# Performance work log

Measured on AMD Instinct MI355X. Metric: run time of the kernel, lower is better.

The kernel has to match this reference:

```python
import jax, jax.numpy as jnp
import numpy as np

TOP_K_FREQ = 16


def setup_inputs() -> dict:
    key = jax.random.key(0)
    x = jax.random.normal(key, (64, 4096, 128), dtype=jnp.float32)
    return {"x": x}


def reference(x):
    B, L, C = x.shape
    freq = jnp.fft.rfft(x, axis=1)              # [B, F, C] complex, F = L//2 + 1
    F = freq.shape[1]
    k = min(TOP_K_FREQ, F)
    mag = jnp.abs(freq)                          # [B, F, C]
    # top-k over frequency axis, vectorized across (B, C)
    mag_bcf = jnp.transpose(mag, (0, 2, 1))      # [B, C, F]
    _, idx = jax.lax.top_k(mag_bcf, k)           # idx: [B, C, k]
    b_ix = jnp.arange(B)[:, None, None]
    c_ix = jnp.arange(C)[None, :, None]
    mask_bcf = jnp.zeros((B, C, F), dtype=x.dtype).at[b_ix, c_ix, idx].set(1.0)
    mask = jnp.transpose(mask_bcf, (0, 2, 1))    # [B, F, C]
    freq_filtered = freq * mask
    out = jnp.fft.irfft(freq_filtered, n=L, axis=1)  # [B, L, C]
    return out.astype(x.dtype)
```

## Files before the change

kernel.cpp:

```cpp
#include <hip/hip_runtime.h>


#define SWZ(i) ((i) ^ (((i) >> 4) & 15))

__device__ __forceinline__ int drev8(int x) {
  return ((x & 7) << 9) | ((x & 0x38) << 3) | ((x >> 3) & 0x38) | ((x >> 9) & 7);
}

__device__ __forceinline__ float2 cmulf(float2 a, float c, float s) {
  return make_float2(a.x * c - a.y * s, a.x * s + a.y * c);
}

__device__ __forceinline__ float2 cadd(float2 a, float2 b) { return make_float2(a.x + b.x, a.y + b.y); }
__device__ __forceinline__ float2 csub(float2 a, float2 b) { return make_float2(a.x - b.x, a.y - b.y); }
__device__ __forceinline__ float2 cmulnegi(float2 a) { return make_float2(a.y, -a.x); }
__device__ __forceinline__ float2 cmulposi(float2 a) { return make_float2(-a.y, a.x); }

__device__ __forceinline__ void dft8(float2* a) {
  const float R = 0.7071067811865476f;
  float2 t0 = cadd(a[0], a[4]), t1 = cadd(a[1], a[5]);
  float2 t2 = cadd(a[2], a[6]), t3 = cadd(a[3], a[7]);
  float2 u0 = csub(a[0], a[4]);
  float2 d1 = csub(a[1], a[5]);
  float2 u1 = make_float2(R * (d1.x + d1.y), R * (d1.y - d1.x));
  float2 u2 = cmulnegi(csub(a[2], a[6]));
  float2 d3 = csub(a[3], a[7]);
  float2 u3 = make_float2(R * (d3.y - d3.x), R * (-(d3.x + d3.y)));
  {
    float2 b0 = cadd(t0, t2), b1 = csub(t0, t2);
    float2 b2 = cadd(t1, t3), b3 = csub(t1, t3);
    a[0] = cadd(b0, b2);
    a[2] = cadd(b1, cmulnegi(b3));
    a[4] = csub(b0, b2);
    a[6] = cadd(b1, cmulposi(b3));
  }
  {
    float2 b0 = cadd(u0, u2), b1 = csub(u0, u2);
    float2 b2 = cadd(u1, u3), b3 = csub(u1, u3);
    a[1] = cadd(b0, b2);
    a[3] = cadd(b1, cmulnegi(b3));
    a[5] = csub(b0, b2);
    a[7] = cadd(b1, cmulposi(b3));
  }
}

template <int STRIDE, int M>
__device__ __forceinline__ void fft_pass8(float2* Zl, int base, int j) {
  float2 v[8];
  #pragma unroll
  for (int p = 0; p < 8; p++) v[p] = Zl[SWZ(base + j + STRIDE * p)];
  dft8(v);
  #pragma unroll
  for (int r = 1; r < 8; r++) {
    if (M > 8) {
      int a = j * r;
      float x = (float)a * (1.0f / (float)M);
      float s = -__builtin_amdgcn_sinf(x);
      float c =  __builtin_amdgcn_cosf(x);
      v[r] = cmulf(v[r], c, s);
    }
  }
  #pragma unroll
  for (int r = 0; r < 8; r++) Zl[SWZ(base + j + STRIDE * r)] = v[r];
}


__global__ __launch_bounds__(512, 8) void fourier_fused(
    const float2* __restrict__ X2, float2* __restrict__ O2) {
  __shared__ float2 Z[4096];
  __shared__ float4 CF[32];
  __shared__ float  CFf[32];

  const int tid = threadIdx.x;
  const int o = ((blockIdx.x & 7) << 9) + (blockIdx.x >> 3);
  const int b = o >> 6;
  const int q = o & 63;

  const float2* src = X2 + (size_t)b * 4096 * 64 + q;
  #pragma unroll
  for (int k = 0; k < 8; k++) {
    int l = tid + 512 * k;
    Z[SWZ(l)] = src[(size_t)l * 64];
  }
  __syncthreads();

  fft_pass8<512, 4096>(Z, 0, tid);
  __syncthreads();
  fft_pass8<64, 512>(Z, (tid >> 6) << 9, tid & 63);
  __syncthreads();
  fft_pass8<8, 64>(Z, (tid >> 3) << 6, tid & 7);
  __syncthreads();
  fft_pass8<1, 8>(Z, tid << 3, 0);
  __syncthreads();

  const int wv = tid >> 6;
  const int lane = tid & 63;

  if (wv < 2) {
    const int ch = wv;
    int rF = 0; float rA = 0.f, rB = 0.f;
    float m2[32];
    #pragma unroll
    for (int k = 0; k < 32; k++) {
      int f = lane + (k << 6);
      float2 P = Z[SWZ(drev8(f))];
      float2 Q = Z[SWZ(drev8((4096 - f) & 4095))];
      float xr = ch ? (P.y + Q.y) : (P.x + Q.x);
      float xi = ch ? (Q.x - P.x) : (P.y - Q.y);
      m2[k] = xr * xr + xi * xi;
    }
    float m2x = -1.f;
    if (lane == 0) {
      float2 P = Z[SWZ(4)];
      float t = ch ? P.y : P.x;
      m2x = 4.f * t * t;
    }
    for (int r = 0; r < 16; r++) {
      float bv = -1e30f; int bf = 0;
      #pragma unroll
      for (int k = 0; k < 32; k++) {
        int f = lane + (k << 6);
        if (m2[k] > bv) { bv = m2[k]; bf = f; }
      }
      if (m2x > bv) { bv = m2x; bf = 2048; }
      #pragma unroll
      for (int off = 32; off; off >>= 1) {
        float ov = __shfl_down(bv, off);
        int   of = __shfl_down(bf, off);
        if (ov > bv || (ov == bv && of < bf)) { bv = ov; bf = of; }
      }
      bf = __shfl(bf, 0);
      if (lane == r) {
        rF = bf;
        float2 P = Z[SWZ(drev8(bf))];
        float2 Q = Z[SWZ(drev8((4096 - bf) & 4095))];
        rA = ch ? 0.5f * (P.y + Q.y) : 0.5f * (P.x + Q.x);
        rB = ch ? 0.5f * (Q.x - P.x) : 0.5f * (P.y - Q.y);
      }
      if (bf == 2048) {
        if (lane == 0) m2x = -2.f;
      } else if ((bf & 63) == lane) {
        int kk = bf >> 6;
        #pragma unroll
        for (int k = 0; k < 32; k++) if (k == kk) m2[k] = -2.f;
      }
    }

    if (lane < 16) {
      const float inv = 2.44140625e-4f;
      float w = (rF == 0 || rF == 2048) ? inv : 2.f * inv;
      float fv = (float)rF;
      float dx = fv * 0.125f;
      dx -= floorf(dx);
      float cd = __builtin_amdgcn_cosf(dx);
      float sd = __builtin_amdgcn_sinf(dx);
      CF[ch * 16 + lane] = make_float4(w * rA, -w * rB, cd, sd);
      CFf[ch * 16 + lane] = fv;
    }
  }
  __syncthreads();

  float* S = (float*)Z;
  const float tf = (float)tid;
  #pragma unroll
  for (int cc = 0; cc < 2; cc++) {
    float u[16], v[16], T[16];
    #pragma unroll
    for (int j = 0; j < 16; j++) {
      float4 cf = CF[cc * 16 + j];
      float f  = CFf[cc * 16 + j];
      float x0 = f * tf * 2.44140625e-4f;
      x0 -= floorf(x0);
      float c0 = __builtin_amdgcn_cosf(x0);
      float s0 = __builtin_amdgcn_sinf(x0);
      float G = fmaf(cf.x, c0, cf.y * s0);
      float H = fmaf(cf.y, c0, -cf.x * s0);
      u[j] = G;
      v[j] = fmaf(G, cf.z, -H * cf.w);
      T[j] = cf.z + cf.z;
    }
    #pragma unroll
    for (int k = 0; k < 8; k += 2) {
      float s0a = 0.f, s1a = 0.f;
      #pragma unroll
      for (int j = 0; j < 16; j++) {
        s0a += u[j];
        v[j] = fmaf(T[j], u[j], -v[j]);
      }
      #pragma unroll
      for (int j = 0; j < 16; j++) {
        s1a += v[j];
        u[j] = fmaf(T[j], v[j], -u[j]);
      }
      S[cc * 4096 + tid + 512 * k]       = s0a;
      S[cc * 4096 + tid + 512 * (k + 1)] = s1a;
    }
  }

  float2* dst = O2 + (size_t)b * 4096 * 64 + q;
  #pragma unroll
  for (int k = 0; k < 8; k++) {
    int l = tid + 512 * k;
    dst[(size_t)l * 64] = make_float2(S[l], S[4096 + l]);
  }
}

extern "C" void kernel_launch(void* const* d_in, const int* in_sizes, int n_in,
                              void* d_out, int out_size, void* d_ws, size_t ws_size,
                              hipStream_t stream) {
  (void)in_sizes; (void)n_in; (void)ws_size; (void)out_size; (void)d_ws;
  const float2* x = (const float2*)d_in[0];
  float2* out = (float2*)d_out;

  fourier_fused<<<dim3(64 * 64), dim3(512), 0, stream>>>(x, out);
}
```

Measured before the change: 596.0 us.

## Process four channels per block with float4 global loads and stores

Each block now handles four channels instead of two. It loads float4 (16-byte) vectors from global memory and keeps the second channel pair in registers while the first pair's FFT and top-k run in shared memory. The synthesis stage accumulates the outputs for all four channels in registers and writes them directly as float4, so the shared-memory staging of results is gone. This targets global-memory access efficiency with wider, more coalesced transactions, at the cost of serialising two FFT passes per block, halving the grid size and raising register pressure (launch bounds lowered to 4 blocks per SM).

```diff
diff --git a/kernel.cpp b/kernel.cpp
--- a/kernel.cpp
+++ b/kernel.cpp
@@ -65,143 +65,162 @@
 }
 
 
-__global__ __launch_bounds__(512, 8) void fourier_fused(
-    const float2* __restrict__ X2, float2* __restrict__ O2) {
+__global__ __launch_bounds__(512, 4) void fourier_fused(
+    const float4* __restrict__ X4, float4* __restrict__ O4) {
   __shared__ float2 Z[4096];
-  __shared__ float4 CF[32];
-  __shared__ float  CFf[32];
+  __shared__ float4 CF[64];
+  __shared__ float  CFf[64];
 
   const int tid = threadIdx.x;
-  const int o = ((blockIdx.x & 7) << 9) + (blockIdx.x >> 3);
-  const int b = o >> 6;
-  const int q = o & 63;
-
-  const float2* src = X2 + (size_t)b * 4096 * 64 + q;
+  const int o = ((blockIdx.x & 7) << 8) + (blockIdx.x >> 3);
+  const int b = o >> 5;
+  const int q = o & 31;
+
+  const int wv = tid >> 6;
+  const int lane = tid & 63;
+
+  const float4* src = X4 + (size_t)b * 4096 * 32 + q;
+  float pr[8], pi[8];
   #pragma unroll
   for (int k = 0; k < 8; k++) {
     int l = tid + 512 * k;
-    Z[SWZ(l)] = src[(size_t)l * 64];
+    float4 v = src[(size_t)l * 32];
+    Z[SWZ(l)] = make_float2(v.x, v.y);
+    pr[k] = v.z;
+    pi[k] = v.w;
   }
   __syncthreads();
 
-  fft_pass8<512, 4096>(Z, 0, tid);
-  __syncthreads();
-  fft_pass8<64, 512>(Z, (tid >> 6) << 9, tid & 63);
-  __syncthreads();
-  fft_pass8<8, 64>(Z, (tid >> 3) << 6, tid & 7);
-  __syncthreads();
-  fft_pass8<1, 8>(Z, tid << 3, 0);
-  __syncthreads();
-
-  const int wv = tid >> 6;
-  const int lane = tid & 63;
-
-  if (wv < 2) {
-    const int ch = wv;
-    int rF = 0; float rA = 0.f, rB = 0.f;
-    float m2[32];
-    #pragma unroll
-    for (int k = 0; k < 32; k++) {
-      int f = lane + (k << 6);
-      float2 P = Z[SWZ(drev8(f))];
-      float2 Q = Z[SWZ(drev8((4096 - f) & 4095))];
-      float xr = ch ? (P.y + Q.y) : (P.x + Q.x);
-      float xi = ch ? (Q.x - P.x) : (P.y - Q.y);
-      m2[k] = xr * xr + xi * xi;
-    }
-    float m2x = -1.f;
-    if (lane == 0) {
-      float2 P = Z[SWZ(4)];
-      float t = ch ? P.y : P.x;
-      m2x = 4.f * t * t;
-    }
-    for (int r = 0; r < 16; r++) {
-      float bv = -1e30f; int bf = 0;
+  #pragma unroll 1
+  for (int half = 0; half < 2; half++) {
+    if (half) {
+      #pragma unroll
+      for (int k = 0; k < 8; k++) Z[SWZ(tid + 512 * k)] = make_float2(pr[k], pi[k]);
+      __syncthreads();
+    }
+
+    fft_pass8<512, 4096>(Z, 0, tid);
+    __syncthreads();
+    fft_pass8<64, 512>(Z, (tid >> 6) << 9, tid & 63);
+    __syncthreads();
+    fft_pass8<8, 64>(Z, (tid >> 3) << 6, tid & 7);
+    __syncthreads();
+    fft_pass8<1, 8>(Z, tid << 3, 0);
+    __syncthreads();
+
+    if (wv < 2) {
+      const int ch = wv;
+      int rF = 0; float rA = 0.f, rB = 0.f;
+      float m2[32];
       #pragma unroll
       for (int k = 0; k < 32; k++) {
         int f = lane + (k << 6);
-        if (m2[k] > bv) { bv = m2[k]; bf = f; }
-      }
-      if (m2x > bv) { bv = m2x; bf = 2048; }
-      #pragma unroll
-      for (int off = 32; off; off >>= 1) {
-        float ov = __shfl_down(bv, off);
-        int   of = __shfl_down(bf, off);
-        if (ov > bv || (ov == bv && of < bf)) { bv = ov; bf = of; }
-      }
-      bf = __shfl(bf, 0);
-      if (lane == r) {
-        rF = bf;
-        float2 P = Z[SWZ(drev8(bf))];
-        float2 Q = Z[SWZ(drev8((4096 - bf) & 4095))];
-        rA = ch ? 0.5f * (P.y + Q.y) : 0.5f * (P.x + Q.x);
-        rB = ch ? 0.5f * (Q.x - P.x) : 0.5f * (P.y - Q.y);
-      }
-      if (bf == 2048) {
-        if (lane == 0) m2x = -2.f;
-      } else if ((bf & 63) == lane) {
-        int kk = bf >> 6;
-        #pragma unroll
-        for (int k = 0; k < 32; k++) if (k == kk) m2[k] = -2.f;
-      }
-    }
-
-    if (lane < 16) {
-      const float inv = 2.44140625e-4f;
-      float w = (rF == 0 || rF == 2048) ? inv : 2.f * inv;
-      float fv = (float)rF;
-      float dx = fv * 0.125f;
-      dx -= floorf(dx);
-      float cd = __builtin_amdgcn_cosf(dx);
-      float sd = __builtin_amdgcn_sinf(dx);
-      CF[ch * 16 + lane] = make_float4(w * rA, -w * rB, cd, sd);
-      CFf[ch * 16 + lane] = fv;
-    }
-  }
-  __syncthreads();
-
-  float* S = (float*)Z;
+        float2 P = Z[SWZ(drev8(f))];
+        float2 Q = Z[SWZ(drev8((4096 - f) & 4095))];
+        float xr = ch ? (P.y + Q.y) : (P.x + Q.x);
+        float xi = ch ? (Q.x - P.x) : (P.y - Q.y);
+        m2[k] = xr * xr + xi * xi;
+      }
+      float m2x = -1.f;
+      if (lane == 0) {
+        float2 P = Z[SWZ(4)];
+        float t = ch ? P.y : P.x;
+        m2x = 4.f * t * t;
+      }
+      for (int r = 0; r < 16; r++) {
+        float bv = -1e30f; int bf = 0;
+        #pragma unroll
+        for (int k = 0; k < 32; k++) {
+          int f = lane + (k << 6);
+          if (m2[k] > bv) { bv = m2[k]; bf = f; }
+        }
+        if (m2x > bv) { bv = m2x; bf = 2048; }
+        #pragma unroll
+        for (int off = 32; off; off >>= 1) {
+          float ov = __shfl_down(bv, off);
+          int   of = __shfl_down(bf, off);
+          if (ov > bv || (ov == bv && of < bf)) { bv = ov; bf = of; }
+        }
+        bf = __shfl(bf, 0);
+        if (lane == r) {
+          rF = bf;
+          float2 P = Z[SWZ(drev8(bf))];
+          float2 Q = Z[SWZ(drev8((4096 - bf) & 4095))];
+          rA = ch ? 0.5f * (P.y + Q.y) : 0.5f * (P.x + Q.x);
+          rB = ch ? 0.5f * (Q.x - P.x) : 0.5f * (P.y - Q.y);
+        }
+        if (bf == 2048) {
+          if (lane == 0) m2x = -2.f;
+        } else if ((bf & 63) == lane) {
+          int kk = bf >> 6;
+          #pragma unroll
+          for (int k = 0; k < 32; k++) if (k == kk) m2[k] = -2.f;
+        }
+      }
+
+      if (lane < 16) {
+        const float inv = 2.44140625e-4f;
+        float w = (rF == 0 || rF == 2048) ? inv : 2.f * inv;
+        float fv = (float)rF;
+        float dx = fv * 0.125f;
+        dx -= floorf(dx);
+        float cd = __builtin_amdgcn_cosf(dx);
+        float sd = __builtin_amdgcn_sinf(dx);
+        int gc = half * 2 + ch;
+        CF[gc * 16 + lane] = make_float4(w * rA, -w * rB, cd, sd);
+        CFf[gc * 16 + lane] = fv;
+      }
+    }
+    __syncthreads();
+  }
+
+  float acc[8][4];
+  #pragma unroll
+  for (int k = 0; k < 8; k++)
+    #pragma unroll
+    for (int c = 0; c < 4; c++) acc[k][c] = 0.f;
+
   const float tf = (float)tid;
   #pragma unroll
-  for (int cc = 0; cc < 2; cc++) {
-    float u[16], v[16], T[16];
-    #pragma unroll
-    for (int j = 0; j < 16; j++) {
-      float4 cf = CF[cc * 16 + j];
-      float f  = CFf[cc * 16 + j];
-      float x0 = f * tf * 2.44140625e-4f;
-      x0 -= floorf(x0);
-      float c0 = __builtin_amdgcn_cosf(x0);
-      float s0 = __builtin_amdgcn_sinf(x0);
-      float G = fmaf(cf.x, c0, cf.y * s0);
-      float H = fmaf(cf.y, c0, -cf.x * s0);
-      u[j] = G;
-      v[j] = fmaf(G, cf.z, -H * cf.w);
-      T[j] = cf.z + cf.z;
-    }
-    #pragma unroll
-    for (int k = 0; k < 8; k += 2) {
-      float s0a = 0.f, s1a = 0.f;
-      #pragma unroll
-      for (int j = 0; j < 16; j++) {
-        s0a += u[j];
-        v[j] = fmaf(T[j], u[j], -v[j]);
-      }
-      #pragma unroll
-      for (int j = 0; j < 16; j++) {
-        s1a += v[j];
-        u[j] = fmaf(T[j], v[j], -u[j]);
-      }
-      S[cc * 4096 + tid + 512 * k]       = s0a;
-      S[cc * 4096 + tid + 512 * (k + 1)] = s1a;
-    }
-  }
-
-  float2* dst = O2 + (size_t)b * 4096 * 64 + q;
+  for (int ch = 0; ch < 4; ch++) {
+    #pragma unroll 1
+    for (int g = 0; g < 4; g++) {
+      float u[4], v[4], T[4];
+      #pragma unroll
+      for (int j = 0; j < 4; j++) {
+        float4 cf = CF[ch * 16 + g * 4 + j];
+        float f  = CFf[ch * 16 + g * 4 + j];
+        float x0 = f * tf * 2.44140625e-4f;
+        x0 -= floorf(x0);
+        float c0 = __builtin_amdgcn_cosf(x0);
+        float s0 = __builtin_amdgcn_sinf(x0);
+        float G = fmaf(cf.x, c0, cf.y * s0);
+        float H = fmaf(cf.y, c0, -cf.x * s0);
+        u[j] = G;
+        v[j] = fmaf(G, cf.z, -H * cf.w);
+        T[j] = cf.z + cf.z;
+      }
+      #pragma unroll
+      for (int k = 0; k < 8; k += 2) {
+        #pragma unroll
+        for (int j = 0; j < 4; j++) {
+          acc[k][ch] += u[j];
+          v[j] = fmaf(T[j], u[j], -v[j]);
+        }
+        #pragma unroll
+        for (int j = 0; j < 4; j++) {
+          acc[k + 1][ch] += v[j];
+          u[j] = fmaf(T[j], v[j], -u[j]);
+        }
+      }
+    }
+  }
+
+  float4* dst = O4 + (size_t)b * 4096 * 32 + q;
   #pragma unroll
   for (int k = 0; k < 8; k++) {
     int l = tid + 512 * k;
-    dst[(size_t)l * 64] = make_float2(S[l], S[4096 + l]);
+    dst[(size_t)l * 32] = make_float4(acc[k][0], acc[k][1], acc[k][2], acc[k][3]);
   }
 }
 
@@ -209,8 +228,8 @@
                               void* d_out, int out_size, void* d_ws, size_t ws_size,
                               hipStream_t stream) {
   (void)in_sizes; (void)n_in; (void)ws_size; (void)out_size; (void)d_ws;
-  const float2* x = (const float2*)d_in[0];
-  float2* out = (float2*)d_out;
-
-  fourier_fused<<<dim3(64 * 64), dim3(512), 0, stream>>>(x, out);
-}
+  const float4* x = (const float4*)d_in[0];
+  float4* out = (float4*)d_out;
+
+  fourier_fused<<<dim3(64 * 32), dim3(512), 0, stream>>>(x, out);
+}
```

New measurement: 954.3 us. 1.6x slower.

## Use half-length complex FFT per channel with 256-thread blocks and shared top-k

Applied to the files above, without the earlier changes.

Each block now handles its two real channels one after the other. Each 4096-point real signal is packed into a 2048-point complex FFT, and the spectrum is recovered through a twiddle post-process. The input for the second channel is parked in registers, shared memory drops to 16 KB, and blocks shrink to 256 threads. Top-k selection now spans four waves and reduces through shared memory, with a barrier on every one of the 16 rounds. Synthesis runs in groups of four frequencies to cut register pressure. The aim is higher occupancy and less LDS per block, paid for with serialised channel processing and extra barriers.

```diff
diff --git a/kernel.cpp b/kernel.cpp
--- a/kernel.cpp
+++ b/kernel.cpp
@@ -3,8 +3,8 @@
 
 #define SWZ(i) ((i) ^ (((i) >> 4) & 15))
 
-__device__ __forceinline__ int drev8(int x) {
-  return ((x & 7) << 9) | ((x & 0x38) << 3) | ((x >> 3) & 0x38) | ((x >> 9) & 7);
+__device__ __forceinline__ int slotOf(int f) {
+  return ((f & 7) << 8) | (((f >> 3) & 7) << 5) | (((f >> 6) & 7) << 2) | ((f >> 9) & 3);
 }
 
 __device__ __forceinline__ float2 cmulf(float2 a, float c, float s) {
@@ -44,6 +44,15 @@
   }
 }
 
+__device__ __forceinline__ void dft4i(float2* a) {
+  float2 t0 = cadd(a[0], a[2]), t1 = csub(a[0], a[2]);
+  float2 t2 = cadd(a[1], a[3]), t3 = csub(a[1], a[3]);
+  a[0] = cadd(t0, t2);
+  a[1] = cadd(t1, cmulnegi(t3));
+  a[2] = csub(t0, t2);
+  a[3] = csub(t1, cmulnegi(t3));
+}
+
 template <int STRIDE, int M>
 __device__ __forceinline__ void fft_pass8(float2* Zl, int base, int j) {
   float2 v[8];
@@ -52,123 +61,37 @@
   dft8(v);
   #pragma unroll
   for (int r = 1; r < 8; r++) {
-    if (M > 8) {
-      int a = j * r;
-      float x = (float)a * (1.0f / (float)M);
-      float s = -__builtin_amdgcn_sinf(x);
-      float c =  __builtin_amdgcn_cosf(x);
-      v[r] = cmulf(v[r], c, s);
-    }
+    int a = j * r;
+    float x = (float)a * (1.0f / (float)M);
+    float s = -__builtin_amdgcn_sinf(x);
+    float c =  __builtin_amdgcn_cosf(x);
+    v[r] = cmulf(v[r], c, s);
   }
   #pragma unroll
   for (int r = 0; r < 8; r++) Zl[SWZ(base + j + STRIDE * r)] = v[r];
 }
 
-
-__global__ __launch_bounds__(512, 8) void fourier_fused(
-    const float2* __restrict__ X2, float2* __restrict__ O2) {
-  __shared__ float2 Z[4096];
-  __shared__ float4 CF[32];
-  __shared__ float  CFf[32];
-
-  const int tid = threadIdx.x;
-  const int o = ((blockIdx.x & 7) << 9) + (blockIdx.x >> 3);
-  const int b = o >> 6;
-  const int q = o & 63;
-
-  const float2* src = X2 + (size_t)b * 4096 * 64 + q;
-  #pragma unroll
-  for (int k = 0; k < 8; k++) {
-    int l = tid + 512 * k;
-    Z[SWZ(l)] = src[(size_t)l * 64];
-  }
-  __syncthreads();
-
-  fft_pass8<512, 4096>(Z, 0, tid);
-  __syncthreads();
-  fft_pass8<64, 512>(Z, (tid >> 6) << 9, tid & 63);
-  __syncthreads();
-  fft_pass8<8, 64>(Z, (tid >> 3) << 6, tid & 7);
-  __syncthreads();
-  fft_pass8<1, 8>(Z, tid << 3, 0);
-  __syncthreads();
-
-  const int wv = tid >> 6;
-  const int lane = tid & 63;
-
-  if (wv < 2) {
-    const int ch = wv;
-    int rF = 0; float rA = 0.f, rB = 0.f;
-    float m2[32];
+__device__ __forceinline__ void fft_pass4x2(float2* Zl, int t) {
+  float2 v[8];
+  #pragma unroll
+  for (int p = 0; p < 8; p++) v[p] = Zl[SWZ(8 * t + p)];
+  dft4i(v);
+  dft4i(v + 4);
+  #pragma unroll
+  for (int p = 0; p < 8; p++) Zl[SWZ(8 * t + p)] = v[p];
+}
+
+__device__ __forceinline__ void synthc(const float4* CF, const float* CFf,
+                                       int cbase, float tf, float* acc) {
+  #pragma unroll
+  for (int k = 0; k < 16; k++) acc[k] = 0.f;
+  #pragma unroll 1
+  for (int g = 0; g < 4; g++) {
+    float u[4], v[4], T[4];
     #pragma unroll
-    for (int k = 0; k < 32; k++) {
-      int f = lane + (k << 6);
-      float2 P = Z[SWZ(drev8(f))];
-      float2 Q = Z[SWZ(drev8((4096 - f) & 4095))];
-      float xr = ch ? (P.y + Q.y) : (P.x + Q.x);
-      float xi = ch ? (Q.x - P.x) : (P.y - Q.y);
-      m2[k] = xr * xr + xi * xi;
-    }
-    float m2x = -1.f;
-    if (lane == 0) {
-      float2 P = Z[SWZ(4)];
-      float t = ch ? P.y : P.x;
-      m2x = 4.f * t * t;
-    }
-    for (int r = 0; r < 16; r++) {
-      float bv = -1e30f; int bf = 0;
-      #pragma unroll
-      for (int k = 0; k < 32; k++) {
-        int f = lane + (k << 6);
-        if (m2[k] > bv) { bv = m2[k]; bf = f; }
-      }
-      if (m2x > bv) { bv = m2x; bf = 2048; }
-      #pragma unroll
-      for (int off = 32; off; off >>= 1) {
-        float ov = __shfl_down(bv, off);
-        int   of = __shfl_down(bf, off);
-        if (ov > bv || (ov == bv && of < bf)) { bv = ov; bf = of; }
-      }
-      bf = __shfl(bf, 0);
-      if (lane == r) {
-        rF = bf;
-        float2 P = Z[SWZ(drev8(bf))];
-        float2 Q = Z[SWZ(drev8((4096 - bf) & 4095))];
-        rA = ch ? 0.5f * (P.y + Q.y) : 0.5f * (P.x + Q.x);
-        rB = ch ? 0.5f * (Q.x - P.x) : 0.5f * (P.y - Q.y);
-      }
-      if (bf == 2048) {
-        if (lane == 0) m2x = -2.f;
-      } else if ((bf & 63) == lane) {
-        int kk = bf >> 6;
-        #pragma unroll
-        for (int k = 0; k < 32; k++) if (k == kk) m2[k] = -2.f;
-      }
-    }
-
-    if (lane < 16) {
-      const float inv = 2.44140625e-4f;
-      float w = (rF == 0 || rF == 2048) ? inv : 2.f * inv;
-      float fv = (float)rF;
-      float dx = fv * 0.125f;
-      dx -= floorf(dx);
-      float cd = __builtin_amdgcn_cosf(dx);
-      float sd = __builtin_amdgcn_sinf(dx);
-      CF[ch * 16 + lane] = make_float4(w * rA, -w * rB, cd, sd);
-      CFf[ch * 16 + lane] = fv;
-    }
-  }
-  __syncthreads();
-
-  float* S = (float*)Z;
-  const float tf = (float)tid;
-  #pragma unroll
-  for (int cc = 0; cc < 2; cc++) {
-    float u[16], v[16], T[16];
-    #pragma unroll
-    for (int j = 0; j < 16; j++) {
-      float4 cf = CF[cc * 16 + j];
-      float f  = CFf[cc * 16 + j];
+    for (int j = 0; j < 4; j++) {
+      float4 cf = CF[cbase + g * 4 + j];
+      float f  = CFf[cbase + g * 4 + j];
       float x0 = f * tf * 2.44140625e-4f;
       x0 -= floorf(x0);
       float c0 = __builtin_amdgcn_cosf(x0);
@@ -180,28 +103,159 @@
       T[j] = cf.z + cf.z;
     }
     #pragma unroll
-    for (int k = 0; k < 8; k += 2) {
-      float s0a = 0.f, s1a = 0.f;
-      #pragma unroll
-      for (int j = 0; j < 16; j++) {
-        s0a += u[j];
-        v[j] = fmaf(T[j], u[j], -v[j]);
-      }
-      #pragma unroll
-      for (int j = 0; j < 16; j++) {
-        s1a += v[j];
-        u[j] = fmaf(T[j], v[j], -u[j]);
-      }
-      S[cc * 4096 + tid + 512 * k]       = s0a;
-      S[cc * 4096 + tid + 512 * (k + 1)] = s1a;
-    }
-  }
+    for (int k = 0; k < 16; k += 2) {
+      #pragma unroll
+      for (int j = 0; j < 4; j++) { acc[k] += u[j];     v[j] = fmaf(T[j], u[j], -v[j]); }
+      #pragma unroll
+      for (int j = 0; j < 4; j++) { acc[k + 1] += v[j]; u[j] = fmaf(T[j], v[j], -u[j]); }
+    }
+  }
+}
+
+
+__global__ __launch_bounds__(256, 4) void fourier_fused(
+    const float2* __restrict__ X2, float2* __restrict__ O2) {
+  __shared__ float2 Z[2048];
+  __shared__ float4 CF[32];
+  __shared__ float  CFf[32];
+  __shared__ float2 TK[4];
+
+  const int tid = threadIdx.x;
+  const int wv = tid >> 6;
+  const int lane = tid & 63;
+  const int o = ((blockIdx.x & 7) << 9) + (blockIdx.x >> 3);
+  const int b = o >> 6;
+  const int q = o & 63;
+
+  float* Zf = (float*)Z;
+  const float inv = 2.44140625e-4f;
+
+  const float2* src = X2 + (size_t)b * 4096 * 64 + q;
+  float park[16];
+  #pragma unroll
+  for (int k = 0; k < 16; k++) {
+    int l = tid + 256 * k;
+    float2 v = src[(size_t)l * 64];
+    Zf[2 * SWZ(l >> 1) + (l & 1)] = v.x;
+    park[k] = v.y;
+  }
+  __syncthreads();
+
+  #pragma unroll 1
+  for (int half = 0; half < 2; half++) {
+    if (half) {
+      #pragma unroll
+      for (int k = 0; k < 16; k++) {
+        int l = tid + 256 * k;
+        Zf[2 * SWZ(l >> 1) + (l & 1)] = park[k];
+      }
+      __syncthreads();
+    }
+
+    fft_pass8<256, 2048>(Z, 0, tid);
+    __syncthreads();
+    fft_pass8<32, 256>(Z, (tid >> 5) << 8, tid & 31);
+    __syncthreads();
+    fft_pass8<4, 32>(Z, (tid >> 2) << 5, tid & 3);
+    __syncthreads();
+    fft_pass4x2(Z, tid);
+    __syncthreads();
+
+    float m2[8];
+    #pragma unroll
+    for (int k = 0; k < 8; k++) {
+      int f = tid + (k << 8);
+      float2 P = Z[SWZ(slotOf(f))];
+      float2 Q = Z[SWZ(slotOf((2048 - f) & 2047))];
+      float x = (float)f * inv;
+      float c = __builtin_amdgcn_cosf(x);
+      float s = __builtin_amdgcn_sinf(x);
+      float Sx = P.x + Q.x, Dy = P.y - Q.y;
+      float Sy = P.y + Q.y, Dx = P.x - Q.x;
+      float xr = Sx + c * Sy - s * Dx;
+      float xi = Dy - c * Dx - s * Sy;
+      m2[k] = xr * xr + xi * xi;
+    }
+    float m2x = -1.f;
+    if (tid == 0) {
+      float2 P = Z[SWZ(0)];
+      float t = P.x - P.y;
+      m2x = 4.f * t * t;
+    }
+
+    for (int r = 0; r < 16; r++) {
+      float bv = -1e30f; int bf = 0;
+      #pragma unroll
+      for (int k = 0; k < 8; k++) {
+        int f = tid + (k << 8);
+        if (m2[k] > bv) { bv = m2[k]; bf = f; }
+      }
+      if (m2x > bv) { bv = m2x; bf = 2048; }
+      #pragma unroll
+      for (int off = 32; off; off >>= 1) {
+        float ov = __shfl_down(bv, off);
+        int   of = __shfl_down(bf, off);
+        if (ov > bv || (ov == bv && of < bf)) { bv = ov; bf = of; }
+      }
+      if (lane == 0) TK[wv] = make_float2(bv, __int_as_float(bf));
+      __syncthreads();
+      bv = TK[0].x; bf = __float_as_int(TK[0].y);
+      #pragma unroll
+      for (int wI = 1; wI < 4; wI++) {
+        float ov = TK[wI].x; int of = __float_as_int(TK[wI].y);
+        if (ov > bv || (ov == bv && of < bf)) { bv = ov; bf = of; }
+      }
+      if (tid == r) {
+        float fv = (float)bf;
+        float alpha, beta;
+        if (bf == 2048) {
+          float2 P = Z[SWZ(0)];
+          alpha = inv * (P.x - P.y);
+          beta = 0.f;
+        } else {
+          float2 P = Z[SWZ(slotOf(bf))];
+          float2 Q = Z[SWZ(slotOf((2048 - bf) & 2047))];
+          float x = fv * inv;
+          float c = __builtin_amdgcn_cosf(x);
+          float s = __builtin_amdgcn_sinf(x);
+          float Sx = P.x + Q.x, Dy = P.y - Q.y;
+          float Sy = P.y + Q.y, Dx = P.x - Q.x;
+          float xr = 0.5f * (Sx + c * Sy - s * Dx);
+          float xi = 0.5f * (Dy - c * Dx - s * Sy);
+          float w = (bf == 0) ? inv : 2.f * inv;
+          alpha = w * xr; beta = -w * xi;
+        }
+        float dxs = fv * 0.0625f;
+        dxs -= floorf(dxs);
+        float cd = __builtin_amdgcn_cosf(dxs);
+        float sd = __builtin_amdgcn_sinf(dxs);
+        CF[(half << 4) + r] = make_float4(alpha, beta, cd, sd);
+        CFf[(half << 4) + r] = fv;
+      }
+      if (bf == 2048) {
+        if (tid == 0) m2x = -2.f;
+      } else if ((bf & 255) == tid) {
+        int kk = bf >> 8;
+        #pragma unroll
+        for (int k = 0; k < 8; k++) if (k == kk) m2[k] = -2.f;
+      }
+      __syncthreads();
+    }
+  }
+
+  float acc[16];
+  const float tf = (float)tid;
+  synthc(CF, CFf, 0, tf, acc);
+  float* Sf = (float*)Z;
+  #pragma unroll
+  for (int k = 0; k < 16; k++) Sf[tid + 256 * k] = acc[k];
+  synthc(CF, CFf, 16, tf, acc);
 
   float2* dst = O2 + (size_t)b * 4096 * 64 + q;
   #pragma unroll
-  for (int k = 0; k < 8; k++) {
-    int l = tid + 512 * k;
-    dst[(size_t)l * 64] = make_float2(S[l], S[4096 + l]);
+  for (int k = 0; k < 16; k++) {
+    int l = tid + 256 * k;
+    dst[(size_t)l * 64] = make_float2(Sf[l], acc[k]);
   }
 }
 
@@ -212,5 +266,5 @@
   const float2* x = (const float2*)d_in[0];
   float2* out = (float2*)d_out;
 
-  fourier_fused<<<dim3(64 * 64), dim3(512), 0, stream>>>(x, out);
-}
+  fourier_fused<<<dim3(64 * 64), dim3(256), 0, stream>>>(x, out);
+}
```

Result: slower. 703.5 us (+18.0%).
